# Kernel tuning notes

Measured on AMD Instinct MI355X. Metric: run time of the kernel, lower is better.

## Reference

```python
import jax, jax.numpy as jnp
import numpy as np
from jax import lax

ML = 3      # mL: intermediate channels of the generated smoother
K = 7       # kernelSize of the generated per-sample kernels
HID = 100   # MLP hidden width


def _conv2d(x, w, pad):
    # x: [N,C,H,W], w: [O,I,kh,kw], 'same'-style padding `pad`
    return lax.conv_general_dilated(
        x, w, window_strides=(1, 1), padding=[(pad, pad), (pad, pad)],
        dimension_numbers=('NCHW', 'OIHW', 'NCHW'))


def _batch_conv2d(inputs, kernels, pad=1):
    # grouped conv trick: inputs [B,1,H,W], kernels [B,1,kh,kw] -> [B,1,H,W]
    B, _, H, W = inputs.shape
    out = lax.conv_general_dilated(
        inputs.reshape(1, B, H, W), kernels, window_strides=(1, 1),
        padding=[(pad, pad), (pad, pad)], feature_group_count=B,
        dimension_numbers=('NCHW', 'OIHW', 'NCHW'))
    return out.reshape(B, 1, H, W)


def setup_inputs() -> dict:
    key = jax.random.key(0)
    ks = jax.random.split(key, 11)
    B, N = 32, 1024
    out_dim = ML * K * K
    inp = {
        'x': jax.random.normal(ks[0], (B, 1, N, N), jnp.float32),
        'f': jax.random.normal(ks[1], (B, 1, N, N), jnp.float32),
        'kernelA': jax.random.normal(ks[2], (B, 1, 3, 3), jnp.float32) * 0.5,
        # fc1: Linear(9,100) -> ReLU -> Linear(100, mL*K*K)   (stored [in,out])
        'fc1_w1': jax.random.normal(ks[3], (9, HID), jnp.float32) / np.sqrt(9.0),
        'fc1_b1': jnp.zeros((HID,), jnp.float32),
        'fc1_w2': jax.random.normal(ks[4], (HID, out_dim), jnp.float32) / np.sqrt(HID),
        'fc1_b2': jnp.zeros((out_dim,), jnp.float32),
        'fc2_w1': jax.random.normal(ks[5], (9, HID), jnp.float32) / np.sqrt(9.0),
        'fc2_b1': jnp.zeros((HID,), jnp.float32),
        'fc2_w2': jax.random.normal(ks[6], (HID, out_dim), jnp.float32) / np.sqrt(HID),
        'fc2_b2': jnp.zeros((out_dim,), jnp.float32),
    }
    return inp


def reference(x, f, kernelA, fc1_w1, fc1_b1, fc1_w2, fc1_b2,
              fc2_w1, fc2_b1, fc2_w2, fc2_b2):
    B = x.shape[0]
    pad = K // 2
    w = kernelA.reshape(B, 9)                                  # flatten(kernelA, 1)
    h1 = jax.nn.relu(w @ fc1_w1 + fc1_b1)
    weight1 = (h1 @ fc1_w2 + fc1_b2).reshape(B, ML, 1, K, K)
    h2 = jax.nn.relu(w @ fc2_w1 + fc2_b1)
    weight2 = (h2 @ fc2_w2 + fc2_b2).reshape(B, 1, ML, K, K)

    Ax = _batch_conv2d(x, kernelA, pad=1)
    r = f - Ax                                                 # residual [B,1,N,N]

    def per_sample(ri, w1, w2):
        # ri: [1,N,N]; w1: [mL,1,K,K]; w2: [1,mL,K,K]
        tmp = _conv2d(ri[None], w1, pad)                       # [1,mL,N,N]
        return _conv2d(tmp, w2, pad)[0]                        # [1,N,N]

    G2 = jax.vmap(per_sample)(r, weight1, weight2)             # [B,1,N,N]
    return x + G2
```

## Files before the change

### kernel.cpp

```cpp
#include <hip/hip_runtime.h>

#define N    1024
#define BSZ  32
#define PS   480
#define HID  100

__global__ __launch_bounds__(256) void prep_kernel(
    const float* __restrict__ kernelA,
    const float* __restrict__ fc1_w1, const float* __restrict__ fc1_b1,
    const float* __restrict__ fc1_w2, const float* __restrict__ fc1_b2,
    const float* __restrict__ fc2_w1, const float* __restrict__ fc2_b1,
    const float* __restrict__ fc2_w2, const float* __restrict__ fc2_b2,
    float* __restrict__ params)
{
    int b = blockIdx.x, t = threadIdx.x;
    __shared__ float w[9], h1[HID], h2[HID], w1[147], w2[147];
    if (t < 9) w[t] = kernelA[b * 9 + t];
    __syncthreads();
    if (t < HID) {
        float s1 = fc1_b1[t], s2 = fc2_b1[t];
        #pragma unroll
        for (int i = 0; i < 9; ++i) {
            s1 = fmaf(w[i], fc1_w1[i * HID + t], s1);
            s2 = fmaf(w[i], fc2_w1[i * HID + t], s2);
        }
        h1[t] = fmaxf(s1, 0.f);
        h2[t] = fmaxf(s2, 0.f);
    }
    __syncthreads();
    if (t < 147) {
        float s1 = fc1_b2[t], s2 = fc2_b2[t];
        for (int i = 0; i < HID; ++i) {
            s1 = fmaf(h1[i], fc1_w2[i * 147 + t], s1);
            s2 = fmaf(h2[i], fc2_w2[i * 147 + t], s2);
        }
        w1[t] = s1;
        w2[t] = s2;
    }
    __syncthreads();
    float* P = params + b * PS;
    if (t < 169) {
        int ey = t / 13, ex = t % 13;
        float s = 0.f;
        for (int m = 0; m < 3; ++m)
            for (int d1y = 0; d1y < 7; ++d1y) {
                int d2y = ey - d1y;
                if (d2y < 0 || d2y > 6) continue;
                for (int d1x = 0; d1x < 7; ++d1x) {
                    int d2x = ex - d1x;
                    if (d2x < 0 || d2x > 6) continue;
                    s = fmaf(w1[m * 49 + d1y * 7 + d1x],
                             w2[m * 49 + d2y * 7 + d2x], s);
                }
            }
        P[t] = s;
    }
    if (t < 147) { P[169 + t] = w1[t]; P[316 + t] = w2[t]; }
    if (t < 9)   P[463 + t] = w[t];
}

#define TR 32
#define TC 128
#define XR 46
#define XC 144
#define RRW 44
#define RC 140
#define NQ 1540

__device__ __forceinline__ void conv_row(const float* win, const float* __restrict__ P,
                                         int ky, float* accRow)
{
    #pragma unroll
    for (int c = 0; c < 13; ++c) {
        float tv = P[ky * 13 + c];
        #pragma unroll
        for (int j = 0; j < 4; ++j)
            accRow[j] = fmaf(win[c + j], tv, accRow[j]);
    }
}

__global__ __launch_bounds__(256, 6) void main_kernel(
    const float* __restrict__ X, const float* __restrict__ F,
    const float* __restrict__ params, float* __restrict__ out)
{
    __shared__ __align__(16) float buf[XR * XC];
    const int t  = threadIdx.x;
    const int b  = blockIdx.z;
    const int y0 = blockIdx.y * TR;
    const int x0 = blockIdx.x * TC;
    const float* P  = params + b * PS;
    const float* Xb = X + (size_t)b * N * N;
    const float* Fb = F + (size_t)b * N * N;
    float*       Ob = out + (size_t)b * N * N;

    for (int idx = t; idx < XR * XC; idx += 256) {
        int i = idx / XC, j = idx - i * XC;
        int gy = y0 - 7 + i, gx = x0 - 7 + j;
        buf[idx] = (gy >= 0 && gy < N && gx >= 0 && gx < N) ? Xb[gy * N + gx] : 0.f;
    }
    __syncthreads();

    float ka[9];
    #pragma unroll
    for (int i = 0; i < 9; ++i) ka[i] = P[463 + i];

    float rq[7][4];
    #pragma unroll
    for (int k = 0; k < 7; ++k) {
        int idx = t + k * 256;
        if (idx < NQ) {
            int i = idx / 35;
            int j = (idx - i * 35) * 4;
            const float* xr = &buf[i * XC + j];
            float s[4] = {0.f, 0.f, 0.f, 0.f};
            #pragma unroll
            for (int dy = 0; dy < 3; ++dy) {
                float w8[8];
                float4 v0 = *reinterpret_cast<const float4*>(xr + dy * XC);
                float4 v1 = *reinterpret_cast<const float4*>(xr + dy * XC + 4);
                w8[0] = v0.x; w8[1] = v0.y; w8[2] = v0.z; w8[3] = v0.w;
                w8[4] = v1.x; w8[5] = v1.y; w8[6] = v1.z; w8[7] = v1.w;
                #pragma unroll
                for (int dx = 0; dx < 3; ++dx)
                    #pragma unroll
                    for (int c = 0; c < 4; ++c)
                        s[c] = fmaf(ka[dy * 3 + dx], w8[dx + c], s[c]);
            }
            int gy = y0 - 6 + i, gxb = x0 - 6 + j;
            #pragma unroll
            for (int c = 0; c < 4; ++c) {
                int gx = gxb + c;
                float v = 0.f;
                if (gy >= 0 && gy < N && gx >= 0 && gx < N)
                    v = Fb[gy * N + gx] - s[c];
                rq[k][c] = v;
            }
        }
    }
    __syncthreads();

    #pragma unroll
    for (int k = 0; k < 7; ++k) {
        int idx = t + k * 256;
        if (idx < NQ) {
            int i = idx / 35;
            int j = (idx - i * 35) * 4;
            float4 v; v.x = rq[k][0]; v.y = rq[k][1]; v.z = rq[k][2]; v.w = rq[k][3];
            *reinterpret_cast<float4*>(&buf[i * RC + j]) = v;
        }
    }
    __syncthreads();

    const int tx4 = (t & 31) * 4;
    const int ty4 = (t >> 5) * 4;
    const float* rbase = &buf[ty4 * RC + tx4];

    float acc[4][4] = {{0.f,0.f,0.f,0.f},{0.f,0.f,0.f,0.f},
                       {0.f,0.f,0.f,0.f},{0.f,0.f,0.f,0.f}};
    float win[16];

    #define LOAD_WIN(rr)                                                     \
        { float4 v0 = *reinterpret_cast<const float4*>(rbase + (rr) * RC);   \
          float4 v1 = *reinterpret_cast<const float4*>(rbase + (rr) * RC + 4);\
          float4 v2 = *reinterpret_cast<const float4*>(rbase + (rr) * RC + 8);\
          float4 v3 = *reinterpret_cast<const float4*>(rbase + (rr) * RC + 12);\
          win[0]=v0.x; win[1]=v0.y; win[2]=v0.z; win[3]=v0.w;                \
          win[4]=v1.x; win[5]=v1.y; win[6]=v1.z; win[7]=v1.w;                \
          win[8]=v2.x; win[9]=v2.y; win[10]=v2.z; win[11]=v2.w;              \
          win[12]=v3.x; win[13]=v3.y; win[14]=v3.z; win[15]=v3.w; }

    LOAD_WIN(0);
    conv_row(win, P, 0, acc[0]);
    LOAD_WIN(1);
    conv_row(win, P, 1, acc[0]);
    conv_row(win, P, 0, acc[1]);
    LOAD_WIN(2);
    conv_row(win, P, 2, acc[0]);
    conv_row(win, P, 1, acc[1]);
    conv_row(win, P, 0, acc[2]);

    for (int rr = 3; rr <= 12; ++rr) {
        LOAD_WIN(rr);
        #pragma unroll
        for (int i = 0; i < 4; ++i)
            conv_row(win, P, rr - i, acc[i]);
    }

    LOAD_WIN(13);
    conv_row(win, P, 12, acc[1]);
    conv_row(win, P, 11, acc[2]);
    conv_row(win, P, 10, acc[3]);
    LOAD_WIN(14);
    conv_row(win, P, 12, acc[2]);
    conv_row(win, P, 11, acc[3]);
    LOAD_WIN(15);
    conv_row(win, P, 12, acc[3]);

    #pragma unroll
    for (int i = 0; i < 4; ++i) {
        const float4 xq = *reinterpret_cast<const float4*>(
            &Xb[(y0 + ty4 + i) * N + (x0 + tx4)]);
        float4 o;
        o.x = xq.x + acc[i][0]; o.y = xq.y + acc[i][1];
        o.z = xq.z + acc[i][2]; o.w = xq.w + acc[i][3];
        *reinterpret_cast<float4*>(&Ob[(y0 + ty4 + i) * N + (x0 + tx4)]) = o;
    }
}

#define SEG 64
#define AXX 14
#define AXU (SEG + 14)
#define ARR 12
#define ARU (SEG + 12)
#define ATA 6
#define ATU (SEG + 6)

__global__ __launch_bounds__(256) void border_kernel(
    const float* __restrict__ X, const float* __restrict__ F,
    const float* __restrict__ params, float* __restrict__ out)
{
    __shared__ float xs[AXX * AXU];
    __shared__ float rs[ARR * ARU];
    __shared__ float tmp[3 * ATA * ATU];
    __shared__ float sw1[147], sw2[147];

    const int  t    = threadIdx.x;
    const int  b    = blockIdx.y;
    const int  seg  = blockIdx.x;
    const int  edge = seg >> 4;
    const int  s    = seg & 15;
    const bool vert = edge >= 2;
    const bool hi   = (edge == 1) || (edge == 3);
    const int  T0   = hi ? (N - 6) : 0;
    const int  V0   = hi ? (N - 3) : 0;
    const int  D    = hi ? 3 : 0;
    const int  u0   = vert ? (3 + s * SEG) : (s * SEG);
    const int  acr0x = T0 - 4, al0x = u0 - 7;
    const int  acr0r = T0 - 3, al0r = u0 - 6;

    const float* P  = params + b * PS;
    const float* Xb = X + (size_t)b * N * N;
    const float* Fb = F + (size_t)b * N * N;
    float*       Ob = out + (size_t)b * N * N;

    if (t < 147) { sw1[t] = P[169 + t]; sw2[t] = P[316 + t]; }
    float ka[9];
    #pragma unroll
    for (int i = 0; i < 9; ++i) ka[i] = P[463 + i];

    for (int idx = t; idx < AXX * AXU; idx += 256) {
        int a = vert ? (idx % AXX) : (idx / AXU);
        int u = vert ? (idx / AXX) : (idx % AXU);
        int ga = acr0x + a, gl = al0x + u;
        int gy = vert ? gl : ga, gx = vert ? ga : gl;
        xs[a * AXU + u] =
            (gy >= 0 && gy < N && gx >= 0 && gx < N) ? Xb[gy * N + gx] : 0.f;
    }
    __syncthreads();

    for (int idx = t; idx < ARR * ARU; idx += 256) {
        int a = vert ? (idx % ARR) : (idx / ARU);
        int u = vert ? (idx / ARR) : (idx % ARU);
        int ga = acr0r + a, gl = al0r + u;
        int gy = vert ? gl : ga, gx = vert ? ga : gl;
        float v = 0.f;
        if (gy >= 0 && gy < N && gx >= 0 && gx < N) {
            float sc = 0.f;
            #pragma unroll
            for (int da = 0; da < 3; ++da)
                #pragma unroll
                for (int dl = 0; dl < 3; ++dl)
                    sc = fmaf(ka[vert ? (dl * 3 + da) : (da * 3 + dl)],
                              xs[(a + da) * AXU + (u + dl)], sc);
            v = Fb[gy * N + gx] - sc;
        }
        rs[a * ARU + u] = v;
    }
    __syncthreads();

    for (int idx = t; idx < 3 * ATA * ATU; idx += 256) {
        int m   = idx / (ATA * ATU);
        int rem = idx - m * (ATA * ATU);
        int a = rem / ATU, u = rem % ATU;
        int gl = (u0 - 3) + u;
        float sc = 0.f;
        if (gl >= 0 && gl < N) {
            #pragma unroll
            for (int da = 0; da < 7; ++da)
                #pragma unroll
                for (int dl = 0; dl < 7; ++dl)
                    sc = fmaf(sw1[m * 49 + (vert ? (dl * 7 + da) : (da * 7 + dl))],
                              rs[(a + da) * ARU + (u + dl)], sc);
        }
        tmp[idx] = sc;
    }
    __syncthreads();

    for (int idx = t; idx < 3 * SEG; idx += 256) {
        int v = idx / SEG, u = idx - (idx / SEG) * SEG;
        int gl = u0 + u, ga = V0 + v;
        if (vert && gl >= N - 3) continue;
        float sc = 0.f;
        #pragma unroll
        for (int m = 0; m < 3; ++m)
            #pragma unroll
            for (int d2a = 0; d2a < 7; ++d2a) {
                int aT = v + d2a - 3 + D;
                if (aT < 0 || aT >= ATA) continue;
                #pragma unroll
                for (int d2l = 0; d2l < 7; ++d2l)
                    sc = fmaf(sw2[m * 49 + (vert ? (d2l * 7 + d2a) : (d2a * 7 + d2l))],
                              tmp[(m * ATA + aT) * ATU + (u + d2l)], sc);
            }
        int gy = vert ? gl : ga, gx = vert ? ga : gl;
        float xv = xs[(ga - acr0x) * AXU + (gl - al0x)];
        Ob[gy * N + gx] = xv + sc;
    }
}

extern "C" void kernel_launch(void* const* d_in, const int* in_sizes, int n_in,
                              void* d_out, int out_size, void* d_ws, size_t ws_size,
                              hipStream_t stream)
{
    const float* x    = (const float*)d_in[0];
    const float* f    = (const float*)d_in[1];
    const float* kA   = (const float*)d_in[2];
    const float* f1w1 = (const float*)d_in[3];
    const float* f1b1 = (const float*)d_in[4];
    const float* f1w2 = (const float*)d_in[5];
    const float* f1b2 = (const float*)d_in[6];
    const float* f2w1 = (const float*)d_in[7];
    const float* f2b1 = (const float*)d_in[8];
    const float* f2w2 = (const float*)d_in[9];
    const float* f2b2 = (const float*)d_in[10];
    float* out    = (float*)d_out;
    float* params = (float*)d_ws;

    prep_kernel<<<BSZ, 256, 0, stream>>>(kA, f1w1, f1b1, f1w2, f1b2,
                                         f2w1, f2b1, f2w2, f2b2, params);
    main_kernel<<<dim3(N / TC, N / TR, BSZ), 256, 0, stream>>>(x, f, params, out);
    border_kernel<<<dim3(64, BSZ), 256, 0, stream>>>(x, f, params, out);
}
```

Before: 542.5 us.

## Double tile height and compute residual straight from global memory

```diff
diff --git a/kernel.cpp b/kernel.cpp
--- a/kernel.cpp
+++ b/kernel.cpp
@@ -59,16 +59,15 @@
     if (t < 9)   P[463 + t] = w[t];
 }
 
-#define TR 32
-#define TC 128
-#define XR 46
-#define XC 144
-#define RRW 44
-#define RC 140
-#define NQ 1540
-
-__device__ __forceinline__ void conv_row(const float* win, const float* __restrict__ P,
-                                         int ky, float* accRow)
+#define TR  64
+#define TC  128
+#define RRW 76
+#define RC  140
+#define QPR 35
+#define NQ  (RRW * QPR)
+
+__device__ __forceinline__ void conv_row4(const float* win, const float* __restrict__ P,
+                                          int ky, float* accRow)
 {
     #pragma unroll
     for (int c = 0; c < 13; ++c) {
@@ -79,11 +78,11 @@
     }
 }
 
-__global__ __launch_bounds__(256, 6) void main_kernel(
+__global__ __launch_bounds__(256, 3) void main_kernel(
     const float* __restrict__ X, const float* __restrict__ F,
     const float* __restrict__ params, float* __restrict__ out)
 {
-    __shared__ __align__(16) float buf[XR * XC];
+    __shared__ __align__(16) float rbuf[RRW * RC];
     const int t  = threadIdx.x;
     const int b  = blockIdx.z;
     const int y0 = blockIdx.y * TR;
@@ -93,117 +92,96 @@
     const float* Fb = F + (size_t)b * N * N;
     float*       Ob = out + (size_t)b * N * N;
 
-    for (int idx = t; idx < XR * XC; idx += 256) {
-        int i = idx / XC, j = idx - i * XC;
-        int gy = y0 - 7 + i, gx = x0 - 7 + j;
-        buf[idx] = (gy >= 0 && gy < N && gx >= 0 && gx < N) ? Xb[gy * N + gx] : 0.f;
-    }
-    __syncthreads();
-
     float ka[9];
     #pragma unroll
     for (int i = 0; i < 9; ++i) ka[i] = P[463 + i];
 
-    float rq[7][4];
-    #pragma unroll
-    for (int k = 0; k < 7; ++k) {
-        int idx = t + k * 256;
-        if (idx < NQ) {
-            int i = idx / 35;
-            int j = (idx - i * 35) * 4;
-            const float* xr = &buf[i * XC + j];
+    for (int idx = t; idx < NQ; idx += 256) {
+        int i  = idx / QPR;
+        int j  = (idx - i * QPR) * 4;
+        int gr = y0 - 6 + i;
+        int gc = x0 - 6 + j;
+        float4 v = make_float4(0.f, 0.f, 0.f, 0.f);
+        if (gr >= 0 && gr < N) {
+            float w8[3][8];
+            #pragma unroll
+            for (int dy = 0; dy < 3; ++dy) {
+                int ry = gr - 1 + dy;
+                float4 qa = make_float4(0.f, 0.f, 0.f, 0.f);
+                float4 qb = make_float4(0.f, 0.f, 0.f, 0.f);
+                if (ry >= 0 && ry < N) {
+                    const float* xr = Xb + (size_t)ry * N;
+                    if (gc - 2 >= 0 && gc + 1 < N)
+                        qa = *reinterpret_cast<const float4*>(xr + gc - 2);
+                    if (gc + 2 >= 0 && gc + 5 < N)
+                        qb = *reinterpret_cast<const float4*>(xr + gc + 2);
+                }
+                w8[dy][0] = qa.x; w8[dy][1] = qa.y; w8[dy][2] = qa.z; w8[dy][3] = qa.w;
+                w8[dy][4] = qb.x; w8[dy][5] = qb.y; w8[dy][6] = qb.z; w8[dy][7] = qb.w;
+            }
             float s[4] = {0.f, 0.f, 0.f, 0.f};
             #pragma unroll
-            for (int dy = 0; dy < 3; ++dy) {
-                float w8[8];
-                float4 v0 = *reinterpret_cast<const float4*>(xr + dy * XC);
-                float4 v1 = *reinterpret_cast<const float4*>(xr + dy * XC + 4);
-                w8[0] = v0.x; w8[1] = v0.y; w8[2] = v0.z; w8[3] = v0.w;
-                w8[4] = v1.x; w8[5] = v1.y; w8[6] = v1.z; w8[7] = v1.w;
+            for (int dy = 0; dy < 3; ++dy)
                 #pragma unroll
-                for (int dx = 0; dx < 3; ++dx)
+                for (int dx = 0; dx < 3; ++dx) {
+                    float kv = ka[dy * 3 + dx];
                     #pragma unroll
                     for (int c = 0; c < 4; ++c)
-                        s[c] = fmaf(ka[dy * 3 + dx], w8[dx + c], s[c]);
-            }
-            int gy = y0 - 6 + i, gxb = x0 - 6 + j;
-            #pragma unroll
-            for (int c = 0; c < 4; ++c) {
-                int gx = gxb + c;
-                float v = 0.f;
-                if (gy >= 0 && gy < N && gx >= 0 && gx < N)
-                    v = Fb[gy * N + gx] - s[c];
-                rq[k][c] = v;
-            }
-        }
-    }
-    __syncthreads();
-
-    #pragma unroll
-    for (int k = 0; k < 7; ++k) {
-        int idx = t + k * 256;
-        if (idx < NQ) {
-            int i = idx / 35;
-            int j = (idx - i * 35) * 4;
-            float4 v; v.x = rq[k][0]; v.y = rq[k][1]; v.z = rq[k][2]; v.w = rq[k][3];
-            *reinterpret_cast<float4*>(&buf[i * RC + j]) = v;
-        }
+                        s[c] = fmaf(kv, w8[dy][c + dx + 1], s[c]);
+                }
+            const float* fr = Fb + (size_t)gr * N;
+            if (gc >= 0 && gc + 1 < N) {
+                float2 f0 = *reinterpret_cast<const float2*>(fr + gc);
+                v.x = f0.x - s[0]; v.y = f0.y - s[1];
+            }
+            if (gc + 2 >= 0 && gc + 3 < N) {
+                float2 f1 = *reinterpret_cast<const float2*>(fr + gc + 2);
+                v.z = f1.x - s[2]; v.w = f1.y - s[3];
+            }
+        }
+        *reinterpret_cast<float4*>(&rbuf[i * RC + j]) = v;
     }
     __syncthreads();
 
     const int tx4 = (t & 31) * 4;
-    const int ty4 = (t >> 5) * 4;
-    const float* rbase = &buf[ty4 * RC + tx4];
-
-    float acc[4][4] = {{0.f,0.f,0.f,0.f},{0.f,0.f,0.f,0.f},
+    const int ty8 = (t >> 5) * 8;
+    const float* rb = &rbuf[ty8 * RC + tx4];
+
+    float acc[8][4] = {{0.f,0.f,0.f,0.f},{0.f,0.f,0.f,0.f},
+                       {0.f,0.f,0.f,0.f},{0.f,0.f,0.f,0.f},
+                       {0.f,0.f,0.f,0.f},{0.f,0.f,0.f,0.f},
                        {0.f,0.f,0.f,0.f},{0.f,0.f,0.f,0.f}};
     float win[16];
 
-    #define LOAD_WIN(rr)                                                     \
-        { float4 v0 = *reinterpret_cast<const float4*>(rbase + (rr) * RC);   \
-          float4 v1 = *reinterpret_cast<const float4*>(rbase + (rr) * RC + 4);\
-          float4 v2 = *reinterpret_cast<const float4*>(rbase + (rr) * RC + 8);\
-          float4 v3 = *reinterpret_cast<const float4*>(rbase + (rr) * RC + 12);\
-          win[0]=v0.x; win[1]=v0.y; win[2]=v0.z; win[3]=v0.w;                \
-          win[4]=v1.x; win[5]=v1.y; win[6]=v1.z; win[7]=v1.w;                \
-          win[8]=v2.x; win[9]=v2.y; win[10]=v2.z; win[11]=v2.w;              \
+    #define LOAD_WIN(rr)                                                      \
+        { float4 v0 = *reinterpret_cast<const float4*>(rb + (rr) * RC);       \
+          float4 v1 = *reinterpret_cast<const float4*>(rb + (rr) * RC + 4);   \
+          float4 v2 = *reinterpret_cast<const float4*>(rb + (rr) * RC + 8);   \
+          float4 v3 = *reinterpret_cast<const float4*>(rb + (rr) * RC + 12);  \
+          win[0]=v0.x; win[1]=v0.y; win[2]=v0.z; win[3]=v0.w;                 \
+          win[4]=v1.x; win[5]=v1.y; win[6]=v1.z; win[7]=v1.w;                 \
+          win[8]=v2.x; win[9]=v2.y; win[10]=v2.z; win[11]=v2.w;               \
           win[12]=v3.x; win[13]=v3.y; win[14]=v3.z; win[15]=v3.w; }
 
-    LOAD_WIN(0);
-    conv_row(win, P, 0, acc[0]);
-    LOAD_WIN(1);
-    conv_row(win, P, 1, acc[0]);
-    conv_row(win, P, 0, acc[1]);
-    LOAD_WIN(2);
-    conv_row(win, P, 2, acc[0]);
-    conv_row(win, P, 1, acc[1]);
-    conv_row(win, P, 0, acc[2]);
-
-    for (int rr = 3; rr <= 12; ++rr) {
+    #pragma unroll
+    for (int rr = 0; rr < 20; ++rr) {
         LOAD_WIN(rr);
+        const int ilo = (rr - 12 > 0) ? rr - 12 : 0;
+        const int ihi = (rr < 7) ? rr : 7;
         #pragma unroll
-        for (int i = 0; i < 4; ++i)
-            conv_row(win, P, rr - i, acc[i]);
-    }
-
-    LOAD_WIN(13);
-    conv_row(win, P, 12, acc[1]);
-    conv_row(win, P, 11, acc[2]);
-    conv_row(win, P, 10, acc[3]);
-    LOAD_WIN(14);
-    conv_row(win, P, 12, acc[2]);
-    conv_row(win, P, 11, acc[3]);
-    LOAD_WIN(15);
-    conv_row(win, P, 12, acc[3]);
-
-    #pragma unroll
-    for (int i = 0; i < 4; ++i) {
+        for (int i = ilo; i <= ihi; ++i)
+            conv_row4(win, P, rr - i, acc[i]);
+    }
+
+    #pragma unroll
+    for (int i = 0; i < 8; ++i) {
+        const int gy = y0 + ty8 + i;
         const float4 xq = *reinterpret_cast<const float4*>(
-            &Xb[(y0 + ty4 + i) * N + (x0 + tx4)]);
+            &Xb[(size_t)gy * N + x0 + tx4]);
         float4 o;
         o.x = xq.x + acc[i][0]; o.y = xq.y + acc[i][1];
         o.z = xq.z + acc[i][2]; o.w = xq.w + acc[i][3];
-        *reinterpret_cast<float4*>(&Ob[(y0 + ty4 + i) * N + (x0 + tx4)]) = o;
+        *reinterpret_cast<float4*>(&Ob[(size_t)gy * N + x0 + tx4]) = o;
     }
 }
 
```

After: 598.9 us. 1.1x slower.
